# Kernel tuning notes

Measured on AMD Instinct MI355X. Metric: run time of the kernel, lower is better.

## Reference

```python
import jax, jax.numpy as jnp
import numpy as np

NUM_HEADS = 16
THETA = 10000.0
B, S, D = 2, 2048, 1024
D_K = D // NUM_HEADS


def setup_inputs() -> dict:
    key = jax.random.key(0)
    ks = jax.random.split(key, 5)
    s = 0.02
    return {
        "x": jax.random.normal(ks[0], (B, S, D), dtype=jnp.float32),
        "W_q": jax.random.normal(ks[1], (D, D), dtype=jnp.float32) * s,
        "W_k": jax.random.normal(ks[2], (D, D), dtype=jnp.float32) * s,
        "W_v": jax.random.normal(ks[3], (D, D), dtype=jnp.float32) * s,
        "W_o": jax.random.normal(ks[4], (D, D), dtype=jnp.float32) * s,
        "token_positions": jnp.arange(S, dtype=jnp.int32),
    }


def _rope(x, token_positions):
    # x: [..., seq, d_k]; equivalent to the block-diagonal 2x2 rotation matmul
    d2 = x.shape[-1] // 2
    inv_freq = THETA ** (-(2.0 * jnp.arange(d2, dtype=x.dtype)) / x.shape[-1])  # [d2]
    ang = token_positions.astype(x.dtype)[:, None] * inv_freq[None, :]  # [seq, d2]
    cos, sin = jnp.cos(ang), jnp.sin(ang)
    xp = x.reshape(x.shape[:-1] + (d2, 2))
    xe, xo = xp[..., 0], xp[..., 1]
    oe = cos * xe - sin * xo
    oo = sin * xe + cos * xo
    return jnp.stack([oe, oo], axis=-1).reshape(x.shape)


def reference(x, W_q, W_k, W_v, W_o, token_positions):
    seq = x.shape[-2]
    # QKV projections (weights stored as [out, in])
    Q = jnp.einsum('bsd,ed->bse', x, W_q)
    K = jnp.einsum('bsd,ed->bse', x, W_k)
    V = jnp.einsum('bsd,ed->bse', x, W_v)
    def split_heads(t):
        return t.reshape(t.shape[:-1] + (NUM_HEADS, D_K)).swapaxes(-3, -2)  # [b,h,s,dk]
    Q, K, V = split_heads(Q), split_heads(K), split_heads(V)
    Q = _rope(Q, token_positions)
    K = _rope(K, token_positions)
    scale = 1.0 / np.sqrt(D_K)
    scores = jnp.einsum('bhqd,bhkd->bhqk', Q, K) * scale
    causal = jnp.tril(jnp.ones((seq, seq), dtype=bool))
    scores = jnp.where(causal, scores, -jnp.inf)
    probs = jax.nn.softmax(scores, axis=-1)
    out = jnp.einsum('bhqk,bhkd->bhqd', probs, V)
    out = out.swapaxes(-3, -2).reshape(x.shape[:-1] + (D,))
    return jnp.einsum('bse,de->bsd', out, W_o)
```

## Files before the change

kernel.cpp:

```cpp
#include <hip/hip_runtime.h>
#include <hip/hip_bf16.h>
#include <math.h>

#define H_    16
#define DK_   64
#define Dm    1024
#define Bb    2
#define Ss    2048
#define Mrows 4096
#define QSCALE 0.1803368801f

typedef short s16x8 __attribute__((ext_vector_type(8)));
typedef float f32x4 __attribute__((ext_vector_type(4)));
typedef unsigned short u16;
typedef unsigned int u32;

__device__ __forceinline__ u16 f2b(float f) {
  __hip_bfloat16 h = __float2bfloat16(f);
  return *reinterpret_cast<u16*>(&h);
}
__device__ __forceinline__ float b2f(u16 u) {
  __hip_bfloat16 h;
  *reinterpret_cast<u16*>(&h) = u;
  return __bfloat162float(h);
}
__device__ __forceinline__ u32 pkbf(float hi, float lo) {
  return __builtin_amdgcn_perm(__float_as_uint(hi), __float_as_uint(lo), 0x07060302u);
}

#define GLDS(g, l)                                                             \
  __builtin_amdgcn_global_load_lds(                                            \
      (const __attribute__((address_space(1))) unsigned int*)(g),              \
      (__attribute__((address_space(3))) unsigned int*)(l), 16, 0, 0)

__device__ __forceinline__ int SW64(int row, int col) {
  return row * 64 + ((((col >> 3) ^ (row & 7) ^ (row >> 3)) & 7) << 3) + (col & 7);
}

__global__ __launch_bounds__(256) void k_castall(
    const float* __restrict__ x,  const float* __restrict__ Wq,
    const float* __restrict__ Wk, const float* __restrict__ Wv,
    const float* __restrict__ Wo,
    u16* __restrict__ xb,  u16* __restrict__ wqb, u16* __restrict__ wkb,
    u16* __restrict__ wvb, u16* __restrict__ wob) {
  int i = blockIdx.x * 256 + threadIdx.x;
  const float* s;
  u16* d;
  int off;
  if (i < 1048576) { s = x; d = xb; off = i; }
  else {
    int j = i - 1048576;
    int w = j >> 18;
    off = j & 262143;
    s = (w == 0) ? Wq : (w == 1) ? Wk : (w == 2) ? Wv : Wo;
    d = (w == 0) ? wqb : (w == 1) ? wkb : (w == 2) ? wvb : wob;
  }
  float4 v = reinterpret_cast<const float4*>(s)[off];
  ushort4 o;
  o.x = f2b(v.x); o.y = f2b(v.y); o.z = f2b(v.z); o.w = f2b(v.w);
  reinterpret_cast<ushort4*>(d)[off] = o;
}

__global__ __launch_bounds__(256) void k_ropetab(const int* __restrict__ pos,
                                                 float2* __restrict__ tab) {
  int t = blockIdx.x * 256 + threadIdx.x;
  int s = t >> 5, i = t & 31;
  float p = (float)pos[s];
  float ang = p * powf(10000.0f, -(float)i / 32.0f);
  tab[t] = make_float2(cosf(ang), sinf(ang));
}

__global__ __launch_bounds__(256) void k_rope2(u16* __restrict__ Q, u16* __restrict__ K,
                                               const float2* __restrict__ tab) {
  int t = blockIdx.x * 256 + threadIdx.x;
  int row = t >> 7;
  int c0 = (t & 127) << 3;
  int i0 = (c0 & 63) >> 1;
  const float2* tb = &tab[(row & (Ss - 1)) * 32 + i0];
  float2 cs[4];
#pragma unroll
  for (int j = 0; j < 4; ++j) cs[j] = tb[j];
  size_t off = (size_t)row * Dm + c0;
  s16x8 q = *reinterpret_cast<const s16x8*>(&Q[off]);
  s16x8 k = *reinterpret_cast<const s16x8*>(&K[off]);
  s16x8 qo, ko;
#pragma unroll
  for (int j = 0; j < 4; ++j) {
    float qe = b2f((u16)q[2 * j]), qd = b2f((u16)q[2 * j + 1]);
    qo[2 * j]     = (short)f2b((cs[j].x * qe - cs[j].y * qd) * QSCALE);
    qo[2 * j + 1] = (short)f2b((cs[j].y * qe + cs[j].x * qd) * QSCALE);
    float ke = b2f((u16)k[2 * j]), kd = b2f((u16)k[2 * j + 1]);
    ko[2 * j]     = (short)f2b(cs[j].x * ke - cs[j].y * kd);
    ko[2 * j + 1] = (short)f2b(cs[j].y * ke + cs[j].x * kd);
  }
  *reinterpret_cast<s16x8*>(&Q[off]) = qo;
  *reinterpret_cast<s16x8*>(&K[off]) = ko;
}

template <int BN>
__global__ __launch_bounds__(256) void k_gemm_bt(
    const u16* __restrict__ A,
    const u16* __restrict__ B0, const u16* __restrict__ B1, const u16* __restrict__ B2,
    u16* __restrict__ O0, u16* __restrict__ O1, u16* __restrict__ OVT,
    float* __restrict__ OF, int M, int N, int K, int f32out) {
  constexpr int NFR = BN / 32;
  __shared__ __align__(16) u16 lsA[128 * 64];
  __shared__ __align__(16) u16 lsB[BN * 64];
  const int tid = threadIdx.x, lane = tid & 63, wave = tid >> 6;
  const int quad = lane >> 4, l16 = lane & 15;
  const int wrow = wave >> 1, wcol = wave & 1;
  const int m0 = blockIdx.x * 128, n0 = blockIdx.y * BN;
  const int z = blockIdx.z;
  const u16* Bp = (z == 0) ? B0 : (z == 1) ? B1 : B2;
  u16* Op = (z == 0) ? O0 : O1;
  f32x4 acc[4][NFR] = {};

  for (int k0 = 0; k0 < K; k0 += 64) {
#pragma unroll
    for (int c = 0; c < 4; ++c) {
      int slot = (wave * 4 + c) * 64 + lane;
      int row = slot >> 3;
      int gg = ((slot & 7) ^ (row & 7) ^ (row >> 3)) & 7;
      GLDS(A + (size_t)(m0 + row) * K + k0 + gg * 8, lsA + (wave * 4 + c) * 512);
    }
#pragma unroll
    for (int c = 0; c < BN / 32; ++c) {
      int cc = wave * (BN / 32) + c;
      int slot = cc * 64 + lane;
      int row = slot >> 3;
      int gg = ((slot & 7) ^ (row & 7) ^ (row >> 3)) & 7;
      GLDS(Bp + (size_t)(n0 + row) * K + k0 + gg * 8, lsB + cc * 512);
    }
    __syncthreads();
#pragma unroll
    for (int kc = 0; kc < 2; ++kc) {
      s16x8 af[4], bfr[NFR];
#pragma unroll
      for (int i = 0; i < 4; ++i)
        af[i] = *reinterpret_cast<const s16x8*>(&lsA[SW64(wrow * 64 + i * 16 + l16, kc * 32 + quad * 8)]);
#pragma unroll
      for (int i = 0; i < NFR; ++i)
        bfr[i] = *reinterpret_cast<const s16x8*>(&lsB[SW64(wcol * (BN / 2) + i * 16 + l16, kc * 32 + quad * 8)]);
#pragma unroll
      for (int mi = 0; mi < 4; ++mi)
#pragma unroll
        for (int ni = 0; ni < NFR; ++ni)
          acc[mi][ni] = __builtin_amdgcn_mfma_f32_16x16x32_bf16(af[mi], bfr[ni], acc[mi][ni], 0, 0, 0);
    }
    __syncthreads();
  }

  if (!f32out && z == 2) {
#pragma unroll
    for (int mi = 0; mi < 4; ++mi)
#pragma unroll
      for (int ni = 0; ni < NFR; ++ni) {
        int row0 = m0 + wrow * 64 + mi * 16 + quad * 4;
        int col  = n0 + wcol * (BN / 2) + ni * 16 + l16;
        int bb = row0 >> 11, s0 = row0 & (Ss - 1);
        ushort4 pk;
        pk.x = f2b(acc[mi][ni][0]); pk.y = f2b(acc[mi][ni][1]);
        pk.z = f2b(acc[mi][ni][2]); pk.w = f2b(acc[mi][ni][3]);
        *reinterpret_cast<ushort4*>(&OVT[((size_t)bb * Dm + col) * Ss + s0]) = pk;
      }
    return;
  }
#pragma unroll
  for (int mi = 0; mi < 4; ++mi)
#pragma unroll
    for (int ni = 0; ni < NFR; ++ni)
#pragma unroll
      for (int r = 0; r < 4; ++r) {
        int row = m0 + wrow * 64 + mi * 16 + quad * 4 + r;
        int col = n0 + wcol * (BN / 2) + ni * 16 + l16;
        float v = acc[mi][ni][r];
        size_t idx = (size_t)row * N + col;
        if (f32out) OF[idx] = v;
        else        Op[idx] = f2b(v);
      }
}

__global__ __launch_bounds__(256) void k_flash(const u16* __restrict__ Q,
                                               const u16* __restrict__ K,
                                               const u16* __restrict__ VT,
                                               u16* __restrict__ O) {
  __shared__ __align__(16) u16 lsK[2][64 * 64];
  __shared__ __align__(16) u16 lsVT[2][64 * 64];
  __shared__ __align__(16) u16 lsP[4][32 * 64];
  const int tid = threadIdx.x, lane = tid & 63, wave = tid >> 6;
  const int quad = lane >> 4, l16 = lane & 15;
  const int bid = blockIdx.x;
  const int bh = bid & 31;
  const int h = bh & (H_ - 1), b = bh >> 4;
  const int g = bid >> 5, a = g & 7, bsel = g >> 3;
  const int qt = bsel ? (15 - a) : a;
  const int q0 = qt * 128;
  const int qbase = q0 + wave * 32;
  const int ktmax_w = (qbase + 31) >> 6;
  const int ktmax_b = 2 * qt + 1;
  const int xorv = (l16 * 2) & 0xE;

  s16x8 qf[2][2];
#pragma unroll
  for (int s = 0; s < 2; ++s) {
    const size_t qoff = (size_t)(b * Ss + qbase + s * 16 + l16) * Dm + h * 64;
    qf[s][0] = *reinterpret_cast<const s16x8*>(&Q[qoff + quad * 8]);
    qf[s][1] = *reinterpret_cast<const s16x8*>(&Q[qoff + 32 + quad * 8]);
  }
  s16x8 ones;
#pragma unroll
  for (int j = 0; j < 8; ++j) ones[j] = (short)0x3F80;

  f32x4 ot[2][4] = {};
  f32x4 lAcc[2] = {};

  auto stage = [&](int kt, int bi) {
    const size_t kbase  = (size_t)(b * Ss + kt * 64) * Dm + h * 64;
    const size_t vtbase = ((size_t)b * Dm + h * 64) * Ss + kt * 64;
#pragma unroll
    for (int c = 0; c < 2; ++c) {
      int slot = (wave * 2 + c) * 64 + lane;
      int row = slot >> 3;
      int gg = ((slot & 7) ^ (row & 7) ^ (row >> 3)) & 7;
      GLDS(K  + kbase  + (size_t)row * Dm + gg * 8, &lsK[bi][(wave * 2 + c) * 512]);
      GLDS(VT + vtbase + (size_t)row * Ss + gg * 8, &lsVT[bi][(wave * 2 + c) * 512]);
    }
  };

  stage(0, 0);
  for (int kt = 0; kt <= ktmax_b; ++kt) {
    __syncthreads();
    if (kt < ktmax_b) stage(kt + 1, (kt + 1) & 1);
    if (kt > ktmax_w) continue;
    const int bi = kt & 1;

    f32x4 st[2][4] = {};
#pragma unroll
    for (int kc = 0; kc < 2; ++kc)
#pragma unroll
      for (int ni = 0; ni < 4; ++ni) {
        s16x8 kf = *reinterpret_cast<const s16x8*>(
            &lsK[bi][SW64(ni * 16 + l16, kc * 32 + quad * 8)]);
        st[0][ni] = __builtin_amdgcn_mfma_f32_16x16x32_bf16(kf, qf[0][kc], st[0][ni], 0, 0, 0);
        st[1][ni] = __builtin_amdgcn_mfma_f32_16x16x32_bf16(kf, qf[1][kc], st[1][ni], 0, 0, 0);
      }
    if (kt == ktmax_w) {
#pragma unroll
      for (int s = 0; s < 2; ++s) {
        int gq = qbase + s * 16 + l16;
#pragma unroll
        for (int ni = 0; ni < 4; ++ni)
#pragma unroll
          for (int r = 0; r < 4; ++r)
            if (kt * 64 + ni * 16 + quad * 4 + r > gq) st[s][ni][r] = -INFINITY;
      }
    }
#pragma unroll
    for (int s = 0; s < 2; ++s)
#pragma unroll
      for (int ni = 0; ni < 4; ++ni) {
        float e0 = __builtin_amdgcn_exp2f(st[s][ni][0]);
        float e1 = __builtin_amdgcn_exp2f(st[s][ni][1]);
        float e2 = __builtin_amdgcn_exp2f(st[s][ni][2]);
        float e3 = __builtin_amdgcn_exp2f(st[s][ni][3]);
        uint2 pk;
        pk.x = pkbf(e1, e0);
        pk.y = pkbf(e3, e2);
        *reinterpret_cast<uint2*>(
            &lsP[wave][(s * 16 + l16) * 64 + (((ni * 4 + quad) ^ xorv) << 2)]) = pk;
      }
#pragma unroll
    for (int kc = 0; kc < 2; ++kc) {
      s16x8 pf0 = *reinterpret_cast<const s16x8*>(
          &lsP[wave][l16 * 64 + (((kc * 8 + quad * 2) ^ xorv) << 2)]);
      s16x8 pf1 = *reinterpret_cast<const s16x8*>(
          &lsP[wave][(16 + l16) * 64 + (((kc * 8 + quad * 2) ^ xorv) << 2)]);
      lAcc[0] = __builtin_amdgcn_mfma_f32_16x16x32_bf16(ones, pf0, lAcc[0], 0, 0, 0);
      lAcc[1] = __builtin_amdgcn_mfma_f32_16x16x32_bf16(ones, pf1, lAcc[1], 0, 0, 0);
#pragma unroll
      for (int ni = 0; ni < 4; ++ni) {
        s16x8 vf = *reinterpret_cast<const s16x8*>(
            &lsVT[bi][SW64(ni * 16 + l16, kc * 32 + quad * 8)]);
        ot[0][ni] = __builtin_amdgcn_mfma_f32_16x16x32_bf16(vf, pf0, ot[0][ni], 0, 0, 0);
        ot[1][ni] = __builtin_amdgcn_mfma_f32_16x16x32_bf16(vf, pf1, ot[1][ni], 0, 0, 0);
      }
    }
  }

#pragma unroll
  for (int s = 0; s < 2; ++s) {
    float inv = 1.0f / lAcc[s][0];
    const size_t obase = (size_t)(b * Ss + qbase + s * 16 + l16) * Dm + h * 64;
#pragma unroll
    for (int ni = 0; ni < 4; ++ni) {
      ushort4 pk;
      pk.x = f2b(ot[s][ni][0] * inv); pk.y = f2b(ot[s][ni][1] * inv);
      pk.z = f2b(ot[s][ni][2] * inv); pk.w = f2b(ot[s][ni][3] * inv);
      *reinterpret_cast<ushort4*>(&O[obase + ni * 16 + quad * 4]) = pk;
    }
  }
}

extern "C" void kernel_launch(void* const* d_in, const int* in_sizes, int n_in,
                              void* d_out, int out_size, void* d_ws, size_t ws_size,
                              hipStream_t stream) {
  const float* x  = (const float*)d_in[0];
  const float* Wq = (const float*)d_in[1];
  const float* Wk = (const float*)d_in[2];
  const float* Wv = (const float*)d_in[3];
  const float* Wo = (const float*)d_in[4];
  const int* pos  = (const int*)d_in[5];
  float* out = (float*)d_out;

  char* w = (char*)d_ws;
  u16* xb  = (u16*)w; w += (size_t)Mrows * Dm * 2;
  u16* wqb = (u16*)w; w += (size_t)Dm * Dm * 2;
  u16* wkb = (u16*)w; w += (size_t)Dm * Dm * 2;
  u16* wvb = (u16*)w; w += (size_t)Dm * Dm * 2;
  u16* wob = (u16*)w; w += (size_t)Dm * Dm * 2;
  u16* Qb  = (u16*)w; w += (size_t)Mrows * Dm * 2;
  u16* Kb  = (u16*)w; w += (size_t)Mrows * Dm * 2;
  u16* VTb = (u16*)w; w += (size_t)Mrows * Dm * 2;
  u16* Ab  = (u16*)w; w += (size_t)Mrows * Dm * 2;
  float2* tabf = (float2*)w; w += (size_t)Ss * 32 * sizeof(float2);

  k_castall<<<8192, 256, 0, stream>>>(x, Wq, Wk, Wv, Wo, xb, wqb, wkb, wvb, wob);
  k_ropetab<<<Ss * 32 / 256, 256, 0, stream>>>(pos, tabf);

  k_gemm_bt<128><<<dim3(32, 8, 3), 256, 0, stream>>>(xb, wqb, wkb, wvb,
                                                     Qb, Kb, VTb, nullptr,
                                                     Mrows, Dm, Dm, 0);
  k_rope2<<<Mrows * Dm / 8 / 256, 256, 0, stream>>>(Qb, Kb, tabf);
  k_flash<<<dim3(512), 256, 0, stream>>>(Qb, Kb, VTb, Ab);
  k_gemm_bt<64><<<dim3(32, 16, 1), 256, 0, stream>>>(Ab, wob, wob, wob,
                                                     nullptr, nullptr, nullptr, out,
                                                     Mrows, Dm, Dm, 1);
}
```

Measured before the change: 202.1 us.

## Double-buffer GEMM LDS tiles and treat QKV as one concatenated-weight GEMM

The GEMM kernel now keeps two LDS buffers and issues the global-to-LDS loads for the next K tile before computing the current one. This overlaps memory latency with MFMA work and drops one barrier per iteration. The QKV projection becomes a single GEMM over a concatenated 3072-row weight (wqb, wkb and wvb are laid out contiguously) with an N-major grid, and the epilogue picks the Q, K or V-transposed output from the column block. The change doubles LDS use, which may lower occupancy, and relies on the three weight buffers being adjacent in the workspace.

Measured after the change: 196.5 us. 1.03x faster.

```diff
diff --git a/kernel.cpp b/kernel.cpp
--- a/kernel.cpp
+++ b/kernel.cpp
@@ -97,87 +97,104 @@
   *reinterpret_cast<s16x8*>(&K[off]) = ko;
 }
 
-template <int BN>
-__global__ __launch_bounds__(256) void k_gemm_bt(
-    const u16* __restrict__ A,
-    const u16* __restrict__ B0, const u16* __restrict__ B1, const u16* __restrict__ B2,
-    u16* __restrict__ O0, u16* __restrict__ O1, u16* __restrict__ OVT,
-    float* __restrict__ OF, int M, int N, int K, int f32out) {
+template <int BN, bool QKV>
+__global__ __launch_bounds__(256) void k_gemm(
+    const u16* __restrict__ A, const u16* __restrict__ B,
+    u16* __restrict__ OQ, u16* __restrict__ OK2, u16* __restrict__ OVT,
+    float* __restrict__ OF, int K) {
   constexpr int NFR = BN / 32;
-  __shared__ __align__(16) u16 lsA[128 * 64];
-  __shared__ __align__(16) u16 lsB[BN * 64];
+  __shared__ __align__(16) u16 lsA[2][128 * 64];
+  __shared__ __align__(16) u16 lsB[2][BN * 64];
   const int tid = threadIdx.x, lane = tid & 63, wave = tid >> 6;
   const int quad = lane >> 4, l16 = lane & 15;
   const int wrow = wave >> 1, wcol = wave & 1;
-  const int m0 = blockIdx.x * 128, n0 = blockIdx.y * BN;
-  const int z = blockIdx.z;
-  const u16* Bp = (z == 0) ? B0 : (z == 1) ? B1 : B2;
-  u16* Op = (z == 0) ? O0 : O1;
+  const int n0 = blockIdx.x * BN, m0 = blockIdx.y * 128;
   f32x4 acc[4][NFR] = {};
 
-  for (int k0 = 0; k0 < K; k0 += 64) {
+  auto stage = [&](int k0, int bi) {
 #pragma unroll
     for (int c = 0; c < 4; ++c) {
       int slot = (wave * 4 + c) * 64 + lane;
       int row = slot >> 3;
       int gg = ((slot & 7) ^ (row & 7) ^ (row >> 3)) & 7;
-      GLDS(A + (size_t)(m0 + row) * K + k0 + gg * 8, lsA + (wave * 4 + c) * 512);
-    }
-#pragma unroll
-    for (int c = 0; c < BN / 32; ++c) {
-      int cc = wave * (BN / 32) + c;
+      GLDS(A + (size_t)(m0 + row) * K + k0 + gg * 8, &lsA[bi][(wave * 4 + c) * 512]);
+    }
+#pragma unroll
+    for (int c = 0; c < NFR; ++c) {
+      int cc = wave * NFR + c;
       int slot = cc * 64 + lane;
       int row = slot >> 3;
       int gg = ((slot & 7) ^ (row & 7) ^ (row >> 3)) & 7;
-      GLDS(Bp + (size_t)(n0 + row) * K + k0 + gg * 8, lsB + cc * 512);
-    }
+      GLDS(B + (size_t)(n0 + row) * K + k0 + gg * 8, &lsB[bi][cc * 512]);
+    }
+  };
+
+  stage(0, 0);
+  int bi = 0;
+  for (int k0 = 0; k0 < K; k0 += 64) {
     __syncthreads();
+    if (k0 + 64 < K) stage(k0 + 64, bi ^ 1);
 #pragma unroll
     for (int kc = 0; kc < 2; ++kc) {
       s16x8 af[4], bfr[NFR];
 #pragma unroll
       for (int i = 0; i < 4; ++i)
-        af[i] = *reinterpret_cast<const s16x8*>(&lsA[SW64(wrow * 64 + i * 16 + l16, kc * 32 + quad * 8)]);
+        af[i] = *reinterpret_cast<const s16x8*>(
+            &lsA[bi][SW64(wrow * 64 + i * 16 + l16, kc * 32 + quad * 8)]);
 #pragma unroll
       for (int i = 0; i < NFR; ++i)
-        bfr[i] = *reinterpret_cast<const s16x8*>(&lsB[SW64(wcol * (BN / 2) + i * 16 + l16, kc * 32 + quad * 8)]);
+        bfr[i] = *reinterpret_cast<const s16x8*>(
+            &lsB[bi][SW64(wcol * (BN / 2) + i * 16 + l16, kc * 32 + quad * 8)]);
 #pragma unroll
       for (int mi = 0; mi < 4; ++mi)
 #pragma unroll
         for (int ni = 0; ni < NFR; ++ni)
           acc[mi][ni] = __builtin_amdgcn_mfma_f32_16x16x32_bf16(af[mi], bfr[ni], acc[mi][ni], 0, 0, 0);
     }
-    __syncthreads();
-  }
-
-  if (!f32out && z == 2) {
+    bi ^= 1;
+  }
+
+  if (QKV) {
+    const int which = n0 >> 10;
+    const int nbase = (n0 & 1023) + wcol * (BN / 2);
+    if (which == 2) {
+#pragma unroll
+      for (int mi = 0; mi < 4; ++mi)
+#pragma unroll
+        for (int ni = 0; ni < NFR; ++ni) {
+          int row0 = m0 + wrow * 64 + mi * 16 + quad * 4;
+          int col  = nbase + ni * 16 + l16;
+          int bb = row0 >> 11, s0 = row0 & (Ss - 1);
+          ushort4 pk;
+          pk.x = f2b(acc[mi][ni][0]); pk.y = f2b(acc[mi][ni][1]);
+          pk.z = f2b(acc[mi][ni][2]); pk.w = f2b(acc[mi][ni][3]);
+          *reinterpret_cast<ushort4*>(&OVT[((size_t)bb * Dm + col) * Ss + s0]) = pk;
+        }
+    } else {
+      u16* Op = which ? OK2 : OQ;
+#pragma unroll
+      for (int mi = 0; mi < 4; ++mi)
+#pragma unroll
+        for (int ni = 0; ni < NFR; ++ni)
+#pragma unroll
+          for (int r = 0; r < 4; ++r) {
+            int row = m0 + wrow * 64 + mi * 16 + quad * 4 + r;
+            int col = nbase + ni * 16 + l16;
+            Op[(size_t)row * Dm + col] = f2b(acc[mi][ni][r]);
+          }
+    }
+  } else {
 #pragma unroll
     for (int mi = 0; mi < 4; ++mi)
 #pragma unroll
-      for (int ni = 0; ni < NFR; ++ni) {
-        int row0 = m0 + wrow * 64 + mi * 16 + quad * 4;
-        int col  = n0 + wcol * (BN / 2) + ni * 16 + l16;
-        int bb = row0 >> 11, s0 = row0 & (Ss - 1);
-        ushort4 pk;
-        pk.x = f2b(acc[mi][ni][0]); pk.y = f2b(acc[mi][ni][1]);
-        pk.z = f2b(acc[mi][ni][2]); pk.w = f2b(acc[mi][ni][3]);
-        *reinterpret_cast<ushort4*>(&OVT[((size_t)bb * Dm + col) * Ss + s0]) = pk;
-      }
-    return;
-  }
-#pragma unroll
-  for (int mi = 0; mi < 4; ++mi)
-#pragma unroll
-    for (int ni = 0; ni < NFR; ++ni)
-#pragma unroll
-      for (int r = 0; r < 4; ++r) {
-        int row = m0 + wrow * 64 + mi * 16 + quad * 4 + r;
-        int col = n0 + wcol * (BN / 2) + ni * 16 + l16;
-        float v = acc[mi][ni][r];
-        size_t idx = (size_t)row * N + col;
-        if (f32out) OF[idx] = v;
-        else        Op[idx] = f2b(v);
-      }
+      for (int ni = 0; ni < NFR; ++ni)
+#pragma unroll
+        for (int r = 0; r < 4; ++r) {
+          int row = m0 + wrow * 64 + mi * 16 + quad * 4 + r;
+          int col = n0 + wcol * (BN / 2) + ni * 16 + l16;
+          OF[(size_t)row * Dm + col] = acc[mi][ni][r];
+        }
+  }
 }
 
 __global__ __launch_bounds__(256) void k_flash(const u16* __restrict__ Q,
@@ -327,12 +344,8 @@
   k_castall<<<8192, 256, 0, stream>>>(x, Wq, Wk, Wv, Wo, xb, wqb, wkb, wvb, wob);
   k_ropetab<<<Ss * 32 / 256, 256, 0, stream>>>(pos, tabf);
 
-  k_gemm_bt<128><<<dim3(32, 8, 3), 256, 0, stream>>>(xb, wqb, wkb, wvb,
-                                                     Qb, Kb, VTb, nullptr,
-                                                     Mrows, Dm, Dm, 0);
+  k_gemm<128, true><<<dim3(24, 32), 256, 0, stream>>>(xb, wqb, Qb, Kb, VTb, nullptr, Dm);
   k_rope2<<<Mrows * Dm / 8 / 256, 256, 0, stream>>>(Qb, Kb, tabf);
   k_flash<<<dim3(512), 256, 0, stream>>>(Qb, Kb, VTb, Ab);
-  k_gemm_bt<64><<<dim3(32, 16, 1), 256, 0, stream>>>(Ab, wob, wob, wob,
-                                                     nullptr, nullptr, nullptr, out,
-                                                     Mrows, Dm, Dm, 1);
-}
+  k_gemm<64, false><<<dim3(16, 32), 256, 0, stream>>>(Ab, wob, nullptr, nullptr, nullptr, out, Dm);
+}
```
